# Kernel optimization log

Measured on AMD Instinct MI355X. Metric: run time of the kernel, lower is better.

## Reference

```python
import jax, jax.numpy as jnp
import numpy as np

B, L, D, E, H = 4, 2048, 512, 8, 1024

def setup_inputs() -> dict:
    key = jax.random.key(0)
    k1, k2, k3, k4 = jax.random.split(key, 4)
    x = jax.random.normal(k1, (B, L, D), dtype=jnp.float32)
    weights = jax.random.uniform(k2, (B, L, E), dtype=jnp.float32)
    w1 = jax.random.normal(k3, (E, D, H), dtype=jnp.float32) * 0.02
    b1 = jnp.zeros((E, H), dtype=jnp.float32)
    w2 = jax.random.normal(k4, (E, H, D), dtype=jnp.float32) * 0.02
    b2 = jnp.zeros((E, D), dtype=jnp.float32)
    return {"x": x, "weights": weights, "w1": w1, "b1": b1, "w2": w2, "b2": b2}

def reference(x, weights, w1, b1, w2, b2):
    # h: [B, L, E, H]
    h = jnp.einsum('bld,edh->bleh', x, w1) + b1[None, None, :, :]
    h = jax.nn.gelu(h, approximate=False)  # torch F.gelu default is exact (erf)
    # out: [B, L, E, D]
    out = jnp.einsum('bleh,ehd->bled', h, w2) + b2[None, None, :, :]
    # weighted sum over experts -> [B, L, D]
    return jnp.einsum('bled,ble->bld', out, weights)
```

## Files before the change

### kernel.cpp

```cpp
#include <hip/hip_runtime.h>
#include <hip/hip_bf16.h>

#define DEV __device__ __forceinline__

typedef __bf16 bf16;
typedef __bf16 bf16x4 __attribute__((ext_vector_type(4)));
typedef __bf16 bf16x8 __attribute__((ext_vector_type(8)));
typedef float f32x4 __attribute__((ext_vector_type(4)));

static constexpr int Bb = 4, Ll = 2048, Dd = 512, Ee = 8, Hh = 1024;
static constexpr int Mm = Bb * Ll;
static constexpr int GKS = Ee * Hh;

DEV void gload_lds16(const void* g, void* l) {
  __builtin_amdgcn_global_load_lds(
      (const __attribute__((address_space(1))) unsigned int*)g,
      (__attribute__((address_space(3))) unsigned int*)l, 16, 0, 0);
}

DEV float gelu_fast(float h) {
  const float k = 0.7978845608028654f * 2.0f * 1.4426950408889634f;
  float h2 = h * h;
  float y = h * (k + (0.044715f * k) * h2);
  float t = exp2f(y);
  return h - h * __frcp_rn(t + 1.0f);
}

__global__ void cvt_x_kernel(const float* __restrict__ in, bf16* __restrict__ out, int n4) {
  int i = blockIdx.x * blockDim.x + threadIdx.x;
  if (i < n4) {
    float4 v = ((const float4*)in)[i];
    bf16x4 o = {(bf16)v.x, (bf16)v.y, (bf16)v.z, (bf16)v.w};
    ((bf16x4*)out)[i] = o;
  }
}

__global__ void transpose_cvt(const float* __restrict__ in, bf16* __restrict__ out,
                              int R, int C, size_t in_es, size_t out_es, int out_rs) {
  __shared__ float tile[64][65];
  const int e = blockIdx.z;
  const float* ip = in + (size_t)e * in_es;
  bf16* op = out + (size_t)e * out_es;
  const int r0 = blockIdx.y * 64, c0 = blockIdx.x * 64;
  const int tc = threadIdx.x & 63, tr = threadIdx.x >> 6;
#pragma unroll
  for (int i = 0; i < 16; ++i) {
    const int r = tr + i * 4;
    tile[r][tc] = ip[(size_t)(r0 + r) * C + c0 + tc];
  }
  __syncthreads();
  const int wr = threadIdx.x & 63, wc0 = threadIdx.x >> 6;
#pragma unroll
  for (int i = 0; i < 16; ++i) {
    const int c = wc0 + i * 4;
    op[(size_t)(c0 + c) * out_rs + r0 + wr] = (bf16)tile[wr][c];
  }
}

template <int ARS, int BRS>
DEV void gemm256_core(const bf16* __restrict__ Ag, const bf16* __restrict__ Bg,
                      int nt, f32x4 (&acc)[8][4], char* lds) {
  const int t = threadIdx.x;
  const int lane = t & 63;
  const int wid = t >> 6;
  const int wm = wid >> 2, wn = wid & 3;
  const int fr = lane & 15, fg = lane >> 4;
  const int srow = t >> 3;
  const int sseg = t & 7;

  auto stage = [&](int kt, int p) {
    char* As = lds + p * 65536;
    char* Bs = lds + p * 65536 + 32768;
#pragma unroll
    for (int i = 0; i < 4; ++i) {
      const int row = i * 64 + srow;
      const int q = sseg ^ (row & 7);
      gload_lds16(Ag + (size_t)row * ARS + kt * 64 + q * 8, As + i * 8192 + wid * 1024);
      gload_lds16(Bg + (size_t)row * BRS + kt * 64 + q * 8, Bs + i * 8192 + wid * 1024);
    }
  };

  stage(0, 0);
  for (int kt = 0; kt < nt; ++kt) {
    const int p = kt & 1;
    if (kt + 1 < nt) {
      stage(kt + 1, p ^ 1);
      asm volatile("s_waitcnt vmcnt(8)" ::: "memory");
    } else {
      asm volatile("s_waitcnt vmcnt(0)" ::: "memory");
    }
    __builtin_amdgcn_s_barrier();
    const char* As = lds + p * 65536;
    const char* Bs = lds + p * 65536 + 32768;
    bf16x8 bfrag[4][2];
#pragma unroll
    for (int q = 0; q < 4; ++q) {
      if (q == 0) {
#pragma unroll
        for (int fj = 0; fj < 4; ++fj)
#pragma unroll
          for (int kk = 0; kk < 2; ++kk) {
            const int row = wn * 64 + fj * 16 + fr;
            const int seg = (kk * 4 + fg) ^ (row & 7);
            bfrag[fj][kk] = *(const bf16x8*)(Bs + row * 128 + seg * 16);
          }
      }
      bf16x8 af[2][2];
#pragma unroll
      for (int fil = 0; fil < 2; ++fil)
#pragma unroll
        for (int kk = 0; kk < 2; ++kk) {
          const int row = wm * 128 + (q * 2 + fil) * 16 + fr;
          const int seg = (kk * 4 + fg) ^ (row & 7);
          af[fil][kk] = *(const bf16x8*)(As + row * 128 + seg * 16);
        }
      __builtin_amdgcn_s_barrier();
      asm volatile("s_waitcnt lgkmcnt(0)" ::: "memory");
      __builtin_amdgcn_sched_barrier(0);
      __builtin_amdgcn_s_setprio(1);
#pragma unroll
      for (int fil = 0; fil < 2; ++fil)
#pragma unroll
        for (int fj = 0; fj < 4; ++fj)
#pragma unroll
          for (int kk = 0; kk < 2; ++kk)
            acc[q * 2 + fil][fj] = __builtin_amdgcn_mfma_f32_16x16x32_bf16(
                bfrag[fj][kk], af[fil][kk], acc[q * 2 + fil][fj], 0, 0, 0);
      __builtin_amdgcn_s_setprio(0);
      __builtin_amdgcn_s_barrier();
    }
  }
}

__global__ __launch_bounds__(512, 2) void ffn_stage1_256(
    const bf16* __restrict__ xb, const bf16* __restrict__ w1t,
    const float* __restrict__ b1, const float* __restrict__ wts,
    bf16* __restrict__ G) {
  __shared__ __align__(16) char lds[131072];
  __shared__ float b1s[256];
  __shared__ float wls[256];
  const int mt = blockIdx.x;
  const int e = blockIdx.y >> 2, ht2 = blockIdx.y & 3;
  const int t = threadIdx.x;
  if (t < 256) b1s[t] = b1[e * Hh + ht2 * 256 + t];
  else wls[t - 256] = wts[((size_t)mt * 256 + (t - 256)) * Ee + e];

  f32x4 acc[8][4] = {};
  const bf16* Ag = xb + (size_t)mt * 256 * Dd;
  const bf16* Bg = w1t + ((size_t)e * Hh + (size_t)ht2 * 256) * Dd;
  gemm256_core<Dd, Dd>(Ag, Bg, Dd / 64, acc, lds);

  const int lane = t & 63, wid = t >> 6;
  const int wm = wid >> 2, wn = wid & 3;
  const int fr = lane & 15, fq = lane >> 4;
  float b1v[4][4];
#pragma unroll
  for (int fj = 0; fj < 4; ++fj)
#pragma unroll
    for (int r = 0; r < 4; ++r) b1v[fj][r] = b1s[wn * 64 + fj * 16 + fq * 4 + r];
#pragma unroll
  for (int fi = 0; fi < 8; ++fi) {
    const int m = mt * 256 + wm * 128 + fi * 16 + fr;
    const float wgt = wls[wm * 128 + fi * 16 + fr];
    bf16* gp = G + (size_t)m * GKS + e * Hh + ht2 * 256 + wn * 64 + fq * 4;
#pragma unroll
    for (int fj = 0; fj < 4; ++fj) {
      bf16x4 o;
#pragma unroll
      for (int r = 0; r < 4; ++r) {
        float v = acc[fi][fj][r] + b1v[fj][r];
        o[r] = (bf16)(gelu_fast(v) * wgt);
      }
      *(bf16x4*)(gp + fj * 16) = o;
    }
  }
}

__global__ __launch_bounds__(512, 2) void ffn_stage2_256(
    const bf16* __restrict__ G, const bf16* __restrict__ w2t,
    float* __restrict__ P, int kchunk) {
  __shared__ __align__(16) char lds[131072];
  const int mt = blockIdx.x, nt = blockIdx.y, s = blockIdx.z;
  f32x4 acc[8][4] = {};
  const bf16* Ag = G + (size_t)mt * 256 * GKS + (size_t)s * kchunk;
  const bf16* Bg = w2t + (size_t)nt * 256 * GKS + (size_t)s * kchunk;
  gemm256_core<GKS, GKS>(Ag, Bg, kchunk / 64, acc, lds);

  float* Pp = P + (size_t)s * Mm * Dd;
  const int t = threadIdx.x;
  const int lane = t & 63, wid = t >> 6;
  const int wm = wid >> 2, wn = wid & 3;
  const int fr = lane & 15, fq = lane >> 4;
#pragma unroll
  for (int fi = 0; fi < 8; ++fi) {
    const size_t m = (size_t)mt * 256 + wm * 128 + fi * 16 + fr;
    float* pp = Pp + m * Dd + nt * 256 + wn * 64 + fq * 4;
#pragma unroll
    for (int fj = 0; fj < 4; ++fj) *(f32x4*)(pp + fj * 16) = acc[fi][fj];
  }
}

__global__ __launch_bounds__(256) void reduce_bias(
    const float* __restrict__ P, const float* __restrict__ wts,
    const float* __restrict__ b2, float* __restrict__ out, int S) {
  const int n4 = Mm * Dd / 4;
  int i = blockIdx.x * 256 + threadIdx.x;
  if (i >= n4) return;
  const int m = i / (Dd / 4);
  const int d0 = (i % (Dd / 4)) * 4;
  float4 a = ((const float4*)P)[i];
  for (int s = 1; s < S; ++s) {
    float4 p = ((const float4*)P)[(size_t)s * n4 + i];
    a.x += p.x; a.y += p.y; a.z += p.z; a.w += p.w;
  }
  const float* wr = wts + (size_t)m * Ee;
#pragma unroll
  for (int e = 0; e < Ee; ++e) {
    const float w = wr[e];
    float4 b = *(const float4*)(b2 + e * Dd + d0);
    a.x += w * b.x; a.y += w * b.y; a.z += w * b.z; a.w += w * b.w;
  }
  ((float4*)out)[i] = a;
}

template <int ARS, int BRS>
DEV void gemm_core(const bf16* __restrict__ Ag, const bf16* __restrict__ Bg,
                   int ksteps, f32x4 (&acc)[4][4], bf16* As, bf16* Bs) {
  const int t = threadIdx.x;
  const int lane = t & 63;
  const int w = t >> 6;
  const int srow = t >> 3;
  const int sseg = t & 7;
  const int wr = w >> 1, wc = w & 1;
  const int fr = lane & 15;
  const int fg = lane >> 4;
  for (int s = 0; s < ksteps; ++s) {
    __syncthreads();
#pragma unroll
    for (int i = 0; i < 4; ++i) {
      const int row = i * 32 + srow;
      const int q = sseg ^ (row & 7);
      gload_lds16(Ag + (size_t)row * ARS + s * 64 + q * 8,
                  (char*)As + i * 4096 + w * 1024);
      gload_lds16(Bg + (size_t)row * BRS + s * 64 + q * 8,
                  (char*)Bs + i * 4096 + w * 1024);
    }
    __syncthreads();
#pragma unroll
    for (int kk = 0; kk < 2; ++kk) {
      bf16x8 af[4], bfr[4];
#pragma unroll
      for (int mi = 0; mi < 4; ++mi) {
        const int row = wr * 64 + mi * 16 + fr;
        const int q = (kk * 4 + fg) ^ (row & 7);
        af[mi] = *(const bf16x8*)((const char*)As + row * 128 + q * 16);
      }
#pragma unroll
      for (int ni = 0; ni < 4; ++ni) {
        const int row = wc * 64 + ni * 16 + fr;
        const int q = (kk * 4 + fg) ^ (row & 7);
        bfr[ni] = *(const bf16x8*)((const char*)Bs + row * 128 + q * 16);
      }
#pragma unroll
      for (int mi = 0; mi < 4; ++mi)
#pragma unroll
        for (int ni = 0; ni < 4; ++ni)
          acc[mi][ni] = __builtin_amdgcn_mfma_f32_16x16x32_bf16(
              af[mi], bfr[ni], acc[mi][ni], 0, 0, 0);
    }
  }
}

__global__ __launch_bounds__(256) void ffn_stage1_t(
    const bf16* __restrict__ xb, const bf16* __restrict__ w1t,
    const float* __restrict__ b1, const float* __restrict__ wts,
    bf16* __restrict__ G) {
  __shared__ __align__(16) bf16 As[128 * 64];
  __shared__ __align__(16) bf16 Bs[128 * 64];
  __shared__ float b1s[128];
  __shared__ float wls[128];
  const int mt = blockIdx.x, ht = blockIdx.y, e = blockIdx.z;
  const int t = threadIdx.x;
  if (t < 128) b1s[t] = b1[e * Hh + ht * 128 + t];
  else wls[t - 128] = wts[((size_t)mt * 128 + (t - 128)) * Ee + e];
  f32x4 acc[4][4] = {};
  const bf16* Ag = xb + (size_t)mt * 128 * Dd;
  const bf16* Bg = w1t + ((size_t)e * Hh + (size_t)ht * 128) * Dd;
  gemm_core<Dd, Dd>(Ag, Bg, Dd / 64, acc, As, Bs);
  const int lane = t & 63, w = t >> 6;
  const int wr = w >> 1, wc = w & 1, fr = lane & 15, fq = lane >> 4;
  float bcol[4];
#pragma unroll
  for (int ni = 0; ni < 4; ++ni) bcol[ni] = b1s[wc * 64 + ni * 16 + fr];
  bf16* gp = G + ((size_t)mt * 128 + wr * 64 + fq * 4) * GKS
               + (size_t)e * Hh + ht * 128 + wc * 64 + fr;
#pragma unroll
  for (int mi = 0; mi < 4; ++mi)
#pragma unroll
    for (int r = 0; r < 4; ++r) {
      const float wgt = wls[wr * 64 + mi * 16 + fq * 4 + r];
#pragma unroll
      for (int ni = 0; ni < 4; ++ni) {
        float v = acc[mi][ni][r] + bcol[ni];
        gp[(size_t)(mi * 16 + r) * GKS + ni * 16] = (bf16)(gelu_fast(v) * wgt);
      }
    }
}

__global__ __launch_bounds__(256) void ffn_stage2_partial(
    const bf16* __restrict__ G, const bf16* __restrict__ w2t,
    float* __restrict__ P, int kchunk) {
  __shared__ __align__(16) bf16 As[128 * 64];
  __shared__ __align__(16) bf16 Bs[128 * 64];
  const int mt = blockIdx.x, nt = blockIdx.y, s = blockIdx.z;
  f32x4 acc[4][4] = {};
  const bf16* Ag = G + (size_t)mt * 128 * GKS + (size_t)s * kchunk;
  const bf16* Bg = w2t + (size_t)nt * 128 * GKS + (size_t)s * kchunk;
  gemm_core<GKS, GKS>(Ag, Bg, kchunk / 64, acc, As, Bs);
  float* Pp = P + (size_t)s * Mm * Dd;
  const int t = threadIdx.x;
  const int lane = t & 63, w = t >> 6;
  const int wr = w >> 1, wc = w & 1, fr = lane & 15, fq = lane >> 4;
#pragma unroll
  for (int mi = 0; mi < 4; ++mi)
#pragma unroll
    for (int r = 0; r < 4; ++r) {
      const size_t m = (size_t)mt * 128 + wr * 64 + mi * 16 + fq * 4 + r;
#pragma unroll
      for (int ni = 0; ni < 4; ++ni) {
        const int d = nt * 128 + wc * 64 + ni * 16 + fr;
        Pp[m * Dd + d] = acc[mi][ni][r];
      }
    }
}

extern "C" void kernel_launch(void* const* d_in, const int* in_sizes, int n_in,
                              void* d_out, int out_size, void* d_ws, size_t ws_size,
                              hipStream_t stream) {
  const float* x   = (const float*)d_in[0];
  const float* wts = (const float*)d_in[1];
  const float* w1  = (const float*)d_in[2];
  const float* b1  = (const float*)d_in[3];
  const float* w2  = (const float*)d_in[4];
  const float* b2  = (const float*)d_in[5];
  float* out = (float*)d_out;

  char* ws = (char*)d_ws;
  size_t off = 0;
  bf16* xb  = (bf16*)(ws + off); off += (size_t)Mm * Dd * 2;
  bf16* w1t = (bf16*)(ws + off); off += (size_t)Ee * Hh * Dd * 2;
  bf16* w2t = (bf16*)(ws + off); off += (size_t)Dd * Ee * Hh * 2;

  const size_t gfull = (size_t)Mm * Ee * Hh * 2;
  const size_t psz   = (size_t)Mm * Dd * 4;

  cvt_x_kernel<<<(Mm * Dd / 4 + 255) / 256, 256, 0, stream>>>(x, xb, Mm * Dd / 4);
  transpose_cvt<<<dim3(Hh / 64, Dd / 64, Ee), 256, 0, stream>>>(
      w1, w1t, Dd, Hh, (size_t)Dd * Hh, (size_t)Hh * Dd, Dd);
  transpose_cvt<<<dim3(Dd / 64, Hh / 64, Ee), 256, 0, stream>>>(
      w2, w2t, Hh, Dd, (size_t)Hh * Dd, (size_t)Hh, Ee * Hh);

  if (ws_size >= off + gfull + 4 * psz) {
    bf16* G = (bf16*)(ws + off);
    float* P = (float*)(ws + off + gfull);
    ffn_stage1_256<<<dim3(Mm / 256, (Ee * Hh) / 256), 512, 0, stream>>>(
        xb, w1t, b1, wts, G);
    ffn_stage2_256<<<dim3(Mm / 256, Dd / 256, 4), 512, 0, stream>>>(
        G, w2t, P, GKS / 4);
    reduce_bias<<<(Mm * Dd / 4 + 255) / 256, 256, 0, stream>>>(P, wts, b2, out, 4);
  } else if (ws_size >= off + gfull + 2 * psz) {
    bf16* G = (bf16*)(ws + off);
    float* P = (float*)(ws + off + gfull);
    ffn_stage1_t<<<dim3(Mm / 128, Hh / 128, Ee), 256, 0, stream>>>(
        xb, w1t, b1, wts, G);
    ffn_stage2_partial<<<dim3(Mm / 128, Dd / 128, 2), 256, 0, stream>>>(
        G, w2t, P, GKS / 2);
    reduce_bias<<<(Mm * Dd / 4 + 255) / 256, 256, 0, stream>>>(P, wts, b2, out, 2);
  }
}
```

Measured before the change: 220.9 us.

## Fuse four H tiles per block in stage1 into one continuous pipelined loop

Stage1 now processes all four 256-wide H tiles of an expert in one block. It runs a single 32-step double-buffered K loop and writes the GELU-weighted epilogue every 8 steps, so the load pipeline keeps going across tile boundaries and the block prologue is amortized. This cuts the grid to a quarter of the blocks, which lowers parallelism and can leave CUs idle. Stage2 inlines the former shared GEMM helper with no behavioural change.

After: 222.2 us. No clear change (+0.6%).

```diff
diff --git a/kernel.cpp b/kernel.cpp
--- a/kernel.cpp
+++ b/kernel.cpp
@@ -57,34 +57,49 @@
   }
 }
 
-template <int ARS, int BRS>
-DEV void gemm256_core(const bf16* __restrict__ Ag, const bf16* __restrict__ Bg,
-                      int nt, f32x4 (&acc)[8][4], char* lds) {
+__global__ __launch_bounds__(512, 2) void ffn_stage1_256(
+    const bf16* __restrict__ xb, const bf16* __restrict__ w1t,
+    const float* __restrict__ b1, const float* __restrict__ wts,
+    bf16* __restrict__ G) {
+  __shared__ __align__(16) char lds[131072];
+  __shared__ float b1s[1024];
+  __shared__ float wls[256];
+  const int mt = blockIdx.x, e = blockIdx.y;
   const int t = threadIdx.x;
+  b1s[t] = b1[e * Hh + t];
+  b1s[512 + t] = b1[e * Hh + 512 + t];
+  if (t < 256) wls[t] = wts[((size_t)mt * 256 + t) * Ee + e];
+
   const int lane = t & 63;
   const int wid = t >> 6;
   const int wm = wid >> 2, wn = wid & 3;
-  const int fr = lane & 15, fg = lane >> 4;
+  const int fr = lane & 15, fg = lane >> 4, fq = lane >> 4;
   const int srow = t >> 3;
   const int sseg = t & 7;
 
-  auto stage = [&](int kt, int p) {
+  const bf16* Ag = xb + (size_t)mt * 256 * Dd;
+  const bf16* Bg0 = w1t + (size_t)e * Hh * Dd;
+
+  auto stage = [&](int it, int p) {
+    const int ht2n = it >> 3, ktn = it & 7;
+    const bf16* Bg = Bg0 + (size_t)ht2n * 256 * Dd;
     char* As = lds + p * 65536;
     char* Bs = lds + p * 65536 + 32768;
 #pragma unroll
     for (int i = 0; i < 4; ++i) {
       const int row = i * 64 + srow;
       const int q = sseg ^ (row & 7);
-      gload_lds16(Ag + (size_t)row * ARS + kt * 64 + q * 8, As + i * 8192 + wid * 1024);
-      gload_lds16(Bg + (size_t)row * BRS + kt * 64 + q * 8, Bs + i * 8192 + wid * 1024);
+      gload_lds16(Ag + (size_t)row * Dd + ktn * 64 + q * 8, As + i * 8192 + wid * 1024);
+      gload_lds16(Bg + (size_t)row * Dd + ktn * 64 + q * 8, Bs + i * 8192 + wid * 1024);
     }
   };
 
+  f32x4 acc[8][4] = {};
   stage(0, 0);
-  for (int kt = 0; kt < nt; ++kt) {
-    const int p = kt & 1;
-    if (kt + 1 < nt) {
-      stage(kt + 1, p ^ 1);
+  for (int it = 0; it < 32; ++it) {
+    const int p = it & 1;
+    if (it + 1 < 32) {
+      stage(it + 1, p ^ 1);
       asm volatile("s_waitcnt vmcnt(8)" ::: "memory");
     } else {
       asm volatile("s_waitcnt vmcnt(0)" ::: "memory");
@@ -129,49 +144,32 @@
       __builtin_amdgcn_s_setprio(0);
       __builtin_amdgcn_s_barrier();
     }
-  }
-}
-
-__global__ __launch_bounds__(512, 2) void ffn_stage1_256(
-    const bf16* __restrict__ xb, const bf16* __restrict__ w1t,
-    const float* __restrict__ b1, const float* __restrict__ wts,
-    bf16* __restrict__ G) {
-  __shared__ __align__(16) char lds[131072];
-  __shared__ float b1s[256];
-  __shared__ float wls[256];
-  const int mt = blockIdx.x;
-  const int e = blockIdx.y >> 2, ht2 = blockIdx.y & 3;
-  const int t = threadIdx.x;
-  if (t < 256) b1s[t] = b1[e * Hh + ht2 * 256 + t];
-  else wls[t - 256] = wts[((size_t)mt * 256 + (t - 256)) * Ee + e];
-
-  f32x4 acc[8][4] = {};
-  const bf16* Ag = xb + (size_t)mt * 256 * Dd;
-  const bf16* Bg = w1t + ((size_t)e * Hh + (size_t)ht2 * 256) * Dd;
-  gemm256_core<Dd, Dd>(Ag, Bg, Dd / 64, acc, lds);
-
-  const int lane = t & 63, wid = t >> 6;
-  const int wm = wid >> 2, wn = wid & 3;
-  const int fr = lane & 15, fq = lane >> 4;
-  float b1v[4][4];
-#pragma unroll
-  for (int fj = 0; fj < 4; ++fj)
-#pragma unroll
-    for (int r = 0; r < 4; ++r) b1v[fj][r] = b1s[wn * 64 + fj * 16 + fq * 4 + r];
-#pragma unroll
-  for (int fi = 0; fi < 8; ++fi) {
-    const int m = mt * 256 + wm * 128 + fi * 16 + fr;
-    const float wgt = wls[wm * 128 + fi * 16 + fr];
-    bf16* gp = G + (size_t)m * GKS + e * Hh + ht2 * 256 + wn * 64 + fq * 4;
-#pragma unroll
-    for (int fj = 0; fj < 4; ++fj) {
-      bf16x4 o;
-#pragma unroll
-      for (int r = 0; r < 4; ++r) {
-        float v = acc[fi][fj][r] + b1v[fj][r];
-        o[r] = (bf16)(gelu_fast(v) * wgt);
-      }
-      *(bf16x4*)(gp + fj * 16) = o;
+    if ((it & 7) == 7) {
+      const int ht2 = it >> 3;
+      float b1v[4][4];
+#pragma unroll
+      for (int fj = 0; fj < 4; ++fj)
+#pragma unroll
+        for (int r = 0; r < 4; ++r)
+          b1v[fj][r] = b1s[ht2 * 256 + wn * 64 + fj * 16 + fq * 4 + r];
+#pragma unroll
+      for (int fi = 0; fi < 8; ++fi) {
+        const int m = mt * 256 + wm * 128 + fi * 16 + fr;
+        const float wgt = wls[wm * 128 + fi * 16 + fr];
+        bf16* gp = G + (size_t)m * GKS + e * Hh + ht2 * 256 + wn * 64 + fq * 4;
+#pragma unroll
+        for (int fj = 0; fj < 4; ++fj) {
+          bf16x4 o;
+#pragma unroll
+          for (int r = 0; r < 4; ++r) {
+            float v = acc[fi][fj][r] + b1v[fj][r];
+            o[r] = (bf16)(gelu_fast(v) * wgt);
+          }
+          *(bf16x4*)(gp + fj * 16) = o;
+        }
+#pragma unroll
+        for (int fj = 0; fj < 4; ++fj) acc[fi][fj] = (f32x4){0.f, 0.f, 0.f, 0.f};
+      }
     }
   }
 }
@@ -181,16 +179,84 @@
     float* __restrict__ P, int kchunk) {
   __shared__ __align__(16) char lds[131072];
   const int mt = blockIdx.x, nt = blockIdx.y, s = blockIdx.z;
-  f32x4 acc[8][4] = {};
+  const int t = threadIdx.x;
+  const int lane = t & 63;
+  const int wid = t >> 6;
+  const int wm = wid >> 2, wn = wid & 3;
+  const int fr = lane & 15, fg = lane >> 4;
+  const int srow = t >> 3;
+  const int sseg = t & 7;
+
   const bf16* Ag = G + (size_t)mt * 256 * GKS + (size_t)s * kchunk;
   const bf16* Bg = w2t + (size_t)nt * 256 * GKS + (size_t)s * kchunk;
-  gemm256_core<GKS, GKS>(Ag, Bg, kchunk / 64, acc, lds);
+
+  auto stage = [&](int kt, int p) {
+    char* As = lds + p * 65536;
+    char* Bs = lds + p * 65536 + 32768;
+#pragma unroll
+    for (int i = 0; i < 4; ++i) {
+      const int row = i * 64 + srow;
+      const int q = sseg ^ (row & 7);
+      gload_lds16(Ag + (size_t)row * GKS + kt * 64 + q * 8, As + i * 8192 + wid * 1024);
+      gload_lds16(Bg + (size_t)row * GKS + kt * 64 + q * 8, Bs + i * 8192 + wid * 1024);
+    }
+  };
+
+  f32x4 acc[8][4] = {};
+  const int nt_k = kchunk / 64;
+  stage(0, 0);
+  for (int kt = 0; kt < nt_k; ++kt) {
+    const int p = kt & 1;
+    if (kt + 1 < nt_k) {
+      stage(kt + 1, p ^ 1);
+      asm volatile("s_waitcnt vmcnt(8)" ::: "memory");
+    } else {
+      asm volatile("s_waitcnt vmcnt(0)" ::: "memory");
+    }
+    __builtin_amdgcn_s_barrier();
+    const char* As = lds + p * 65536;
+    const char* Bs = lds + p * 65536 + 32768;
+    bf16x8 bfrag[4][2];
+#pragma unroll
+    for (int q = 0; q < 4; ++q) {
+      if (q == 0) {
+#pragma unroll
+        for (int fj = 0; fj < 4; ++fj)
+#pragma unroll
+          for (int kk = 0; kk < 2; ++kk) {
+            const int row = wn * 64 + fj * 16 + fr;
+            const int seg = (kk * 4 + fg) ^ (row & 7);
+            bfrag[fj][kk] = *(const bf16x8*)(Bs + row * 128 + seg * 16);
+          }
+      }
+      bf16x8 af[2][2];
+#pragma unroll
+      for (int fil = 0; fil < 2; ++fil)
+#pragma unroll
+        for (int kk = 0; kk < 2; ++kk) {
+          const int row = wm * 128 + (q * 2 + fil) * 16 + fr;
+          const int seg = (kk * 4 + fg) ^ (row & 7);
+          af[fil][kk] = *(const bf16x8*)(As + row * 128 + seg * 16);
+        }
+      __builtin_amdgcn_s_barrier();
+      asm volatile("s_waitcnt lgkmcnt(0)" ::: "memory");
+      __builtin_amdgcn_sched_barrier(0);
+      __builtin_amdgcn_s_setprio(1);
+#pragma unroll
+      for (int fil = 0; fil < 2; ++fil)
+#pragma unroll
+        for (int fj = 0; fj < 4; ++fj)
+#pragma unroll
+          for (int kk = 0; kk < 2; ++kk)
+            acc[q * 2 + fil][fj] = __builtin_amdgcn_mfma_f32_16x16x32_bf16(
+                bfrag[fj][kk], af[fil][kk], acc[q * 2 + fil][fj], 0, 0, 0);
+      __builtin_amdgcn_s_setprio(0);
+      __builtin_amdgcn_s_barrier();
+    }
+  }
 
   float* Pp = P + (size_t)s * Mm * Dd;
-  const int t = threadIdx.x;
-  const int lane = t & 63, wid = t >> 6;
-  const int wm = wid >> 2, wn = wid & 3;
-  const int fr = lane & 15, fq = lane >> 4;
+  const int fq = lane >> 4;
 #pragma unroll
   for (int fi = 0; fi < 8; ++fi) {
     const size_t m = (size_t)mt * 256 + wm * 128 + fi * 16 + fr;
@@ -363,7 +429,7 @@
   if (ws_size >= off + gfull + 4 * psz) {
     bf16* G = (bf16*)(ws + off);
     float* P = (float*)(ws + off + gfull);
-    ffn_stage1_256<<<dim3(Mm / 256, (Ee * Hh) / 256), 512, 0, stream>>>(
+    ffn_stage1_256<<<dim3(Mm / 256, Ee), 512, 0, stream>>>(
         xb, w1t, b1, wts, G);
     ffn_stage2_256<<<dim3(Mm / 256, Dd / 256, 4), 512, 0, stream>>>(
         G, w2t, P, GKS / 4);
```

## Shrink GEMM tiles to 256x128 with K=32 steps for higher occupancy

Applied to the files above, without the earlier changes.

Replaces the 256x256 tile, K=64 GEMM core with a 256x128 tile and K=32 stages, using 8 waves in a 4x2 layout. Each wave now holds a 64x64 accumulator, and LDS use drops from 128KB to 48KB per block, so launch bounds are raised to 4 blocks per CU and the grids double along N. The aim is more blocks in flight and more latency hiding. In exchange, each tile reuses less data, global/LDS traffic per FLOP goes up, and there are more barriers per unit of K.

Measured after the change: 227.3 us. +2.9%, slower.

```diff
diff --git a/kernel.cpp b/kernel.cpp
--- a/kernel.cpp
+++ b/kernel.cpp
@@ -58,100 +58,88 @@
 }
 
 template <int ARS, int BRS>
-DEV void gemm256_core(const bf16* __restrict__ Ag, const bf16* __restrict__ Bg,
-                      int nt, f32x4 (&acc)[8][4], char* lds) {
+DEV void gemm128_run(const bf16* __restrict__ Ag, const bf16* __restrict__ Bg,
+                     int nt_k, f32x4 (&acc)[4][4], char* lds) {
   const int t = threadIdx.x;
   const int lane = t & 63;
   const int wid = t >> 6;
-  const int wm = wid >> 2, wn = wid & 3;
+  const int wm = wid >> 1, wn = wid & 1;
   const int fr = lane & 15, fg = lane >> 4;
-  const int srow = t >> 3;
-  const int sseg = t & 7;
+  const int srow = t >> 2;
+  const int sseg = t & 3;
 
   auto stage = [&](int kt, int p) {
-    char* As = lds + p * 65536;
-    char* Bs = lds + p * 65536 + 32768;
-#pragma unroll
-    for (int i = 0; i < 4; ++i) {
-      const int row = i * 64 + srow;
-      const int q = sseg ^ (row & 7);
-      gload_lds16(Ag + (size_t)row * ARS + kt * 64 + q * 8, As + i * 8192 + wid * 1024);
-      gload_lds16(Bg + (size_t)row * BRS + kt * 64 + q * 8, Bs + i * 8192 + wid * 1024);
+    char* As = lds + p * 24576;
+    char* Bs = lds + p * 24576 + 16384;
+#pragma unroll
+    for (int i = 0; i < 2; ++i) {
+      const int row = i * 128 + srow;
+      const int q = sseg ^ (row & 3);
+      gload_lds16(Ag + (size_t)row * ARS + kt * 32 + q * 8, As + i * 8192 + wid * 1024);
+    }
+    {
+      const int row = srow;
+      const int q = sseg ^ (row & 3);
+      gload_lds16(Bg + (size_t)row * BRS + kt * 32 + q * 8, Bs + wid * 1024);
     }
   };
 
   stage(0, 0);
-  for (int kt = 0; kt < nt; ++kt) {
+  for (int kt = 0; kt < nt_k; ++kt) {
     const int p = kt & 1;
-    if (kt + 1 < nt) {
+    if (kt + 1 < nt_k) {
       stage(kt + 1, p ^ 1);
-      asm volatile("s_waitcnt vmcnt(8)" ::: "memory");
+      asm volatile("s_waitcnt vmcnt(3)" ::: "memory");
     } else {
       asm volatile("s_waitcnt vmcnt(0)" ::: "memory");
     }
     __builtin_amdgcn_s_barrier();
-    const char* As = lds + p * 65536;
-    const char* Bs = lds + p * 65536 + 32768;
-    bf16x8 bfrag[4][2];
-#pragma unroll
-    for (int q = 0; q < 4; ++q) {
-      if (q == 0) {
-#pragma unroll
-        for (int fj = 0; fj < 4; ++fj)
-#pragma unroll
-          for (int kk = 0; kk < 2; ++kk) {
-            const int row = wn * 64 + fj * 16 + fr;
-            const int seg = (kk * 4 + fg) ^ (row & 7);
-            bfrag[fj][kk] = *(const bf16x8*)(Bs + row * 128 + seg * 16);
-          }
-      }
-      bf16x8 af[2][2];
-#pragma unroll
-      for (int fil = 0; fil < 2; ++fil)
-#pragma unroll
-        for (int kk = 0; kk < 2; ++kk) {
-          const int row = wm * 128 + (q * 2 + fil) * 16 + fr;
-          const int seg = (kk * 4 + fg) ^ (row & 7);
-          af[fil][kk] = *(const bf16x8*)(As + row * 128 + seg * 16);
-        }
-      __builtin_amdgcn_s_barrier();
-      asm volatile("s_waitcnt lgkmcnt(0)" ::: "memory");
-      __builtin_amdgcn_sched_barrier(0);
-      __builtin_amdgcn_s_setprio(1);
-#pragma unroll
-      for (int fil = 0; fil < 2; ++fil)
-#pragma unroll
-        for (int fj = 0; fj < 4; ++fj)
-#pragma unroll
-          for (int kk = 0; kk < 2; ++kk)
-            acc[q * 2 + fil][fj] = __builtin_amdgcn_mfma_f32_16x16x32_bf16(
-                bfrag[fj][kk], af[fil][kk], acc[q * 2 + fil][fj], 0, 0, 0);
-      __builtin_amdgcn_s_setprio(0);
-      __builtin_amdgcn_s_barrier();
-    }
-  }
-}
-
-__global__ __launch_bounds__(512, 2) void ffn_stage1_256(
+    const char* As = lds + p * 24576;
+    const char* Bs = lds + p * 24576 + 16384;
+    bf16x8 bfr[4], af[4];
+#pragma unroll
+    for (int fj = 0; fj < 4; ++fj) {
+      const int row = wn * 64 + fj * 16 + fr;
+      const int s = fg ^ (row & 3);
+      bfr[fj] = *(const bf16x8*)(Bs + row * 64 + s * 16);
+    }
+#pragma unroll
+    for (int fi = 0; fi < 4; ++fi) {
+      const int row = wm * 64 + fi * 16 + fr;
+      const int s = fg ^ (row & 3);
+      af[fi] = *(const bf16x8*)(As + row * 64 + s * 16);
+    }
+    __builtin_amdgcn_s_setprio(1);
+#pragma unroll
+    for (int fi = 0; fi < 4; ++fi)
+#pragma unroll
+      for (int fj = 0; fj < 4; ++fj)
+        acc[fi][fj] = __builtin_amdgcn_mfma_f32_16x16x32_bf16(
+            bfr[fj], af[fi], acc[fi][fj], 0, 0, 0);
+    __builtin_amdgcn_s_setprio(0);
+    __builtin_amdgcn_s_barrier();
+  }
+}
+
+__global__ __launch_bounds__(512, 4) void ffn_stage1_256(
     const bf16* __restrict__ xb, const bf16* __restrict__ w1t,
     const float* __restrict__ b1, const float* __restrict__ wts,
     bf16* __restrict__ G) {
-  __shared__ __align__(16) char lds[131072];
-  __shared__ float b1s[256];
+  __shared__ __align__(16) char lds[49152];
+  __shared__ float b1s[128];
   __shared__ float wls[256];
-  const int mt = blockIdx.x;
-  const int e = blockIdx.y >> 2, ht2 = blockIdx.y & 3;
-  const int t = threadIdx.x;
-  if (t < 256) b1s[t] = b1[e * Hh + ht2 * 256 + t];
-  else wls[t - 256] = wts[((size_t)mt * 256 + (t - 256)) * Ee + e];
-
-  f32x4 acc[8][4] = {};
+  const int mt = blockIdx.x, ct = blockIdx.y;
+  const int t = threadIdx.x;
+  if (t < 128) b1s[t] = b1[ct * 128 + t];
+  else if (t < 384) wls[t - 128] = wts[((size_t)mt * 256 + (t - 128)) * Ee + (ct >> 3)];
+
+  f32x4 acc[4][4] = {};
   const bf16* Ag = xb + (size_t)mt * 256 * Dd;
-  const bf16* Bg = w1t + ((size_t)e * Hh + (size_t)ht2 * 256) * Dd;
-  gemm256_core<Dd, Dd>(Ag, Bg, Dd / 64, acc, lds);
+  const bf16* Bg = w1t + (size_t)ct * 128 * Dd;
+  gemm128_run<Dd, Dd>(Ag, Bg, Dd / 32, acc, lds);
 
   const int lane = t & 63, wid = t >> 6;
-  const int wm = wid >> 2, wn = wid & 3;
+  const int wm = wid >> 1, wn = wid & 1;
   const int fr = lane & 15, fq = lane >> 4;
   float b1v[4][4];
 #pragma unroll
@@ -159,10 +147,10 @@
 #pragma unroll
     for (int r = 0; r < 4; ++r) b1v[fj][r] = b1s[wn * 64 + fj * 16 + fq * 4 + r];
 #pragma unroll
-  for (int fi = 0; fi < 8; ++fi) {
-    const int m = mt * 256 + wm * 128 + fi * 16 + fr;
-    const float wgt = wls[wm * 128 + fi * 16 + fr];
-    bf16* gp = G + (size_t)m * GKS + e * Hh + ht2 * 256 + wn * 64 + fq * 4;
+  for (int fi = 0; fi < 4; ++fi) {
+    const int m = mt * 256 + wm * 64 + fi * 16 + fr;
+    const float wgt = wls[wm * 64 + fi * 16 + fr];
+    bf16* gp = G + (size_t)m * GKS + ct * 128 + wn * 64 + fq * 4;
 #pragma unroll
     for (int fj = 0; fj < 4; ++fj) {
       bf16x4 o;
@@ -176,25 +164,26 @@
   }
 }
 
-__global__ __launch_bounds__(512, 2) void ffn_stage2_256(
+__global__ __launch_bounds__(512, 4) void ffn_stage2_256(
     const bf16* __restrict__ G, const bf16* __restrict__ w2t,
     float* __restrict__ P, int kchunk) {
-  __shared__ __align__(16) char lds[131072];
+  __shared__ __align__(16) char lds[49152];
   const int mt = blockIdx.x, nt = blockIdx.y, s = blockIdx.z;
-  f32x4 acc[8][4] = {};
+  const int t = threadIdx.x;
+
+  f32x4 acc[4][4] = {};
   const bf16* Ag = G + (size_t)mt * 256 * GKS + (size_t)s * kchunk;
-  const bf16* Bg = w2t + (size_t)nt * 256 * GKS + (size_t)s * kchunk;
-  gemm256_core<GKS, GKS>(Ag, Bg, kchunk / 64, acc, lds);
+  const bf16* Bg = w2t + (size_t)nt * 128 * GKS + (size_t)s * kchunk;
+  gemm128_run<GKS, GKS>(Ag, Bg, kchunk / 32, acc, lds);
 
   float* Pp = P + (size_t)s * Mm * Dd;
-  const int t = threadIdx.x;
   const int lane = t & 63, wid = t >> 6;
-  const int wm = wid >> 2, wn = wid & 3;
+  const int wm = wid >> 1, wn = wid & 1;
   const int fr = lane & 15, fq = lane >> 4;
 #pragma unroll
-  for (int fi = 0; fi < 8; ++fi) {
-    const size_t m = (size_t)mt * 256 + wm * 128 + fi * 16 + fr;
-    float* pp = Pp + m * Dd + nt * 256 + wn * 64 + fq * 4;
+  for (int fi = 0; fi < 4; ++fi) {
+    const size_t m = (size_t)mt * 256 + wm * 64 + fi * 16 + fr;
+    float* pp = Pp + m * Dd + nt * 128 + wn * 64 + fq * 4;
 #pragma unroll
     for (int fj = 0; fj < 4; ++fj) *(f32x4*)(pp + fj * 16) = acc[fi][fj];
   }
@@ -363,9 +352,9 @@
   if (ws_size >= off + gfull + 4 * psz) {
     bf16* G = (bf16*)(ws + off);
     float* P = (float*)(ws + off + gfull);
-    ffn_stage1_256<<<dim3(Mm / 256, (Ee * Hh) / 256), 512, 0, stream>>>(
+    ffn_stage1_256<<<dim3(Mm / 256, GKS / 128), 512, 0, stream>>>(
         xb, w1t, b1, wts, G);
-    ffn_stage2_256<<<dim3(Mm / 256, Dd / 256, 4), 512, 0, stream>>>(
+    ffn_stage2_256<<<dim3(Mm / 256, Dd / 128, 4), 512, 0, stream>>>(
         G, w2t, P, GKS / 4);
     reduce_bias<<<(Mm * Dd / 4 + 255) / 256, 256, 0, stream>>>(P, wts, b2, out, 4);
   } else if (ws_size >= off + gfull + 2 * psz) {
```

## Restructure GEMM pipeline to triple-buffered K=32 stages with interleaved loads

Applied to the files above, without the earlier changes.

Replaces the shared double-buffered K=64 GEMM core with a triple-buffered K=32 pipeline. The next tile's A and B global-to-LDS loads are issued between the two MFMA clusters, and the LDS swizzle is changed to match the narrower rows. Stage 1 now has each block loop over all four 256-wide H tiles of one expert in a single persistent loop, writing the GELU epilogue every 16 iterations. This cuts the grid from 1024 to 256 blocks and lets the pipeline run without a drain between tiles. Launch bounds drop from 2 to 1 block per CU, trading occupancy for deeper prefetch and fewer load stalls.

Result: no change. 223.9 us (+1.3%).

```diff
diff --git a/kernel.cpp b/kernel.cpp
--- a/kernel.cpp
+++ b/kernel.cpp
@@ -57,140 +57,168 @@
   }
 }
 
-template <int ARS, int BRS>
-DEV void gemm256_core(const bf16* __restrict__ Ag, const bf16* __restrict__ Bg,
-                      int nt, f32x4 (&acc)[8][4], char* lds) {
-  const int t = threadIdx.x;
-  const int lane = t & 63;
-  const int wid = t >> 6;
-  const int wm = wid >> 2, wn = wid & 3;
-  const int fr = lane & 15, fg = lane >> 4;
-  const int srow = t >> 3;
-  const int sseg = t & 7;
-
-  auto stage = [&](int kt, int p) {
-    char* As = lds + p * 65536;
-    char* Bs = lds + p * 65536 + 32768;
-#pragma unroll
-    for (int i = 0; i < 4; ++i) {
-      const int row = i * 64 + srow;
-      const int q = sseg ^ (row & 7);
-      gload_lds16(Ag + (size_t)row * ARS + kt * 64 + q * 8, As + i * 8192 + wid * 1024);
-      gload_lds16(Bg + (size_t)row * BRS + kt * 64 + q * 8, Bs + i * 8192 + wid * 1024);
-    }
-  };
-
-  stage(0, 0);
-  for (int kt = 0; kt < nt; ++kt) {
-    const int p = kt & 1;
-    if (kt + 1 < nt) {
-      stage(kt + 1, p ^ 1);
-      asm volatile("s_waitcnt vmcnt(8)" ::: "memory");
-    } else {
-      asm volatile("s_waitcnt vmcnt(0)" ::: "memory");
-    }
-    __builtin_amdgcn_s_barrier();
-    const char* As = lds + p * 65536;
-    const char* Bs = lds + p * 65536 + 32768;
-    bf16x8 bfrag[4][2];
-#pragma unroll
-    for (int q = 0; q < 4; ++q) {
-      if (q == 0) {
-#pragma unroll
-        for (int fj = 0; fj < 4; ++fj)
-#pragma unroll
-          for (int kk = 0; kk < 2; ++kk) {
-            const int row = wn * 64 + fj * 16 + fr;
-            const int seg = (kk * 4 + fg) ^ (row & 7);
-            bfrag[fj][kk] = *(const bf16x8*)(Bs + row * 128 + seg * 16);
-          }
-      }
-      bf16x8 af[2][2];
-#pragma unroll
-      for (int fil = 0; fil < 2; ++fil)
-#pragma unroll
-        for (int kk = 0; kk < 2; ++kk) {
-          const int row = wm * 128 + (q * 2 + fil) * 16 + fr;
-          const int seg = (kk * 4 + fg) ^ (row & 7);
-          af[fil][kk] = *(const bf16x8*)(As + row * 128 + seg * 16);
-        }
-      __builtin_amdgcn_s_barrier();
-      asm volatile("s_waitcnt lgkmcnt(0)" ::: "memory");
-      __builtin_amdgcn_sched_barrier(0);
-      __builtin_amdgcn_s_setprio(1);
-#pragma unroll
-      for (int fil = 0; fil < 2; ++fil)
-#pragma unroll
-        for (int fj = 0; fj < 4; ++fj)
-#pragma unroll
-          for (int kk = 0; kk < 2; ++kk)
-            acc[q * 2 + fil][fj] = __builtin_amdgcn_mfma_f32_16x16x32_bf16(
-                bfrag[fj][kk], af[fil][kk], acc[q * 2 + fil][fj], 0, 0, 0);
-      __builtin_amdgcn_s_setprio(0);
-      __builtin_amdgcn_s_barrier();
-    }
-  }
-}
-
-__global__ __launch_bounds__(512, 2) void ffn_stage1_256(
+#define PIPE_DECLS                                                   \
+  const int t = threadIdx.x;                                         \
+  const int lane = t & 63;                                           \
+  const int wid = t >> 6;                                            \
+  const int wm = wid >> 2, wn = wid & 3;                             \
+  const int fr = lane & 15, fg = lane >> 4, fq = lane >> 4;          \
+  const int srow = t >> 2;                                           \
+  const int sq = (t & 3) ^ ((t >> 3) & 3);                           \
+  const int rsl = fg ^ ((fr >> 1) & 3);
+
+#define PHASE0(buf)                                                  \
+  bf16x8 bfr[4], af[4];                                              \
+  _Pragma("unroll") for (int fj = 0; fj < 4; ++fj) {                 \
+    const int row = wn * 64 + fj * 16 + fr;                          \
+    bfr[fj] = *(const bf16x8*)((buf) + 16384 + row * 64 + rsl * 16); \
+  }                                                                  \
+  _Pragma("unroll") for (int fi = 0; fi < 4; ++fi) {                 \
+    const int row = wm * 128 + fi * 16 + fr;                         \
+    af[fi] = *(const bf16x8*)((buf) + row * 64 + rsl * 16);          \
+  }
+
+#define PHASE1_READS(buf)                                            \
+  bf16x8 af2[4];                                                     \
+  _Pragma("unroll") for (int fi = 0; fi < 4; ++fi) {                 \
+    const int row = wm * 128 + (4 + fi) * 16 + fr;                   \
+    af2[fi] = *(const bf16x8*)((buf) + row * 64 + rsl * 16);         \
+  }
+
+#define MFMA_CLUSTER(A, ACCOFF)                                      \
+  __builtin_amdgcn_s_barrier();                                      \
+  asm volatile("s_waitcnt lgkmcnt(0)" ::: "memory");                 \
+  __builtin_amdgcn_sched_barrier(0);                                 \
+  __builtin_amdgcn_s_setprio(1);                                     \
+  _Pragma("unroll") for (int fi = 0; fi < 4; ++fi)                   \
+  _Pragma("unroll") for (int fj = 0; fj < 4; ++fj)                   \
+    acc[(ACCOFF) + fi][fj] = __builtin_amdgcn_mfma_f32_16x16x32_bf16(\
+        bfr[fj], (A)[fi], acc[(ACCOFF) + fi][fj], 0, 0, 0);          \
+  __builtin_amdgcn_s_setprio(0);
+
+__global__ __launch_bounds__(512, 1) void ffn_stage1_f(
     const bf16* __restrict__ xb, const bf16* __restrict__ w1t,
     const float* __restrict__ b1, const float* __restrict__ wts,
     bf16* __restrict__ G) {
-  __shared__ __align__(16) char lds[131072];
-  __shared__ float b1s[256];
+  __shared__ __align__(16) char lds[98304];
+  __shared__ float b1s[1024];
   __shared__ float wls[256];
-  const int mt = blockIdx.x;
-  const int e = blockIdx.y >> 2, ht2 = blockIdx.y & 3;
-  const int t = threadIdx.x;
-  if (t < 256) b1s[t] = b1[e * Hh + ht2 * 256 + t];
-  else wls[t - 256] = wts[((size_t)mt * 256 + (t - 256)) * Ee + e];
+  const int mt = blockIdx.x, e = blockIdx.y;
+  PIPE_DECLS
+  b1s[t] = b1[e * Hh + t];
+  b1s[512 + t] = b1[e * Hh + 512 + t];
+  if (t < 256) wls[t] = wts[((size_t)mt * 256 + t) * Ee + e];
+
+  const bf16* Ag = xb + (size_t)mt * 256 * Dd;
+  const bf16* Bg0 = w1t + (size_t)e * Hh * Dd;
+
+  auto stageA = [&](int it, char* buf) {
+    const int k0 = (it & 15) * 32;
+    gload_lds16(Ag + (size_t)srow * Dd + k0 + sq * 8, buf + wid * 1024);
+    gload_lds16(Ag + (size_t)(128 + srow) * Dd + k0 + sq * 8, buf + 8192 + wid * 1024);
+  };
+  auto stageB = [&](int it, char* buf) {
+    const bf16* Bg = Bg0 + (size_t)(it >> 4) * 256 * Dd;
+    const int k0 = (it & 15) * 32;
+    gload_lds16(Bg + (size_t)srow * Dd + k0 + sq * 8, buf + 16384 + wid * 1024);
+    gload_lds16(Bg + (size_t)(128 + srow) * Dd + k0 + sq * 8, buf + 24576 + wid * 1024);
+  };
 
   f32x4 acc[8][4] = {};
-  const bf16* Ag = xb + (size_t)mt * 256 * Dd;
-  const bf16* Bg = w1t + ((size_t)e * Hh + (size_t)ht2 * 256) * Dd;
-  gemm256_core<Dd, Dd>(Ag, Bg, Dd / 64, acc, lds);
-
-  const int lane = t & 63, wid = t >> 6;
-  const int wm = wid >> 2, wn = wid & 3;
-  const int fr = lane & 15, fq = lane >> 4;
-  float b1v[4][4];
-#pragma unroll
-  for (int fj = 0; fj < 4; ++fj)
-#pragma unroll
-    for (int r = 0; r < 4; ++r) b1v[fj][r] = b1s[wn * 64 + fj * 16 + fq * 4 + r];
-#pragma unroll
-  for (int fi = 0; fi < 8; ++fi) {
-    const int m = mt * 256 + wm * 128 + fi * 16 + fr;
-    const float wgt = wls[wm * 128 + fi * 16 + fr];
-    bf16* gp = G + (size_t)m * GKS + e * Hh + ht2 * 256 + wn * 64 + fq * 4;
-#pragma unroll
-    for (int fj = 0; fj < 4; ++fj) {
-      bf16x4 o;
-#pragma unroll
-      for (int r = 0; r < 4; ++r) {
-        float v = acc[fi][fj][r] + b1v[fj][r];
-        o[r] = (bf16)(gelu_fast(v) * wgt);
+  const int NT = 64;
+  stageA(0, lds); stageB(0, lds);
+  stageA(1, lds + 32768); stageB(1, lds + 32768);
+  for (int it = 0; it < NT; ++it) {
+    char* buf = lds + (it % 3) * 32768;
+    char* nbuf = lds + ((it + 2) % 3) * 32768;
+    if (it + 1 < NT) {
+      asm volatile("s_waitcnt vmcnt(4)" ::: "memory");
+    } else {
+      asm volatile("s_waitcnt vmcnt(0)" ::: "memory");
+    }
+    __builtin_amdgcn_s_barrier();
+    {
+      PHASE0(buf)
+      if (it + 2 < NT) stageA(it + 2, nbuf);
+      MFMA_CLUSTER(af, 0)
+      PHASE1_READS(buf)
+      if (it + 2 < NT) stageB(it + 2, nbuf);
+      MFMA_CLUSTER(af2, 4)
+    }
+    if ((it & 15) == 15) {
+      const int ct = it >> 4;
+      float b1v[4][4];
+#pragma unroll
+      for (int fj = 0; fj < 4; ++fj)
+#pragma unroll
+        for (int r = 0; r < 4; ++r)
+          b1v[fj][r] = b1s[ct * 256 + wn * 64 + fj * 16 + fq * 4 + r];
+#pragma unroll
+      for (int fi = 0; fi < 8; ++fi) {
+        const int m = mt * 256 + wm * 128 + fi * 16 + fr;
+        const float wgt = wls[wm * 128 + fi * 16 + fr];
+        bf16* gp = G + (size_t)m * GKS + e * Hh + ct * 256 + wn * 64 + fq * 4;
+#pragma unroll
+        for (int fj = 0; fj < 4; ++fj) {
+          bf16x4 o;
+#pragma unroll
+          for (int r = 0; r < 4; ++r) {
+            float v = acc[fi][fj][r] + b1v[fj][r];
+            o[r] = (bf16)(gelu_fast(v) * wgt);
+          }
+          *(bf16x4*)(gp + fj * 16) = o;
+#pragma unroll
+          for (int r = 0; r < 4; ++r) acc[fi][fj][r] = 0.f;
+        }
       }
-      *(bf16x4*)(gp + fj * 16) = o;
-    }
-  }
-}
-
-__global__ __launch_bounds__(512, 2) void ffn_stage2_256(
+    }
+  }
+}
+
+__global__ __launch_bounds__(512, 1) void ffn_stage2_f(
     const bf16* __restrict__ G, const bf16* __restrict__ w2t,
-    float* __restrict__ P, int kchunk) {
-  __shared__ __align__(16) char lds[131072];
+    float* __restrict__ P) {
+  __shared__ __align__(16) char lds[98304];
   const int mt = blockIdx.x, nt = blockIdx.y, s = blockIdx.z;
+  PIPE_DECLS
+  const bf16* Ag = G + (size_t)mt * 256 * GKS + (size_t)s * 2048;
+  const bf16* Bg = w2t + (size_t)nt * 256 * GKS + (size_t)s * 2048;
+
+  auto stageA = [&](int it, char* buf) {
+    const int k0 = it * 32;
+    gload_lds16(Ag + (size_t)srow * GKS + k0 + sq * 8, buf + wid * 1024);
+    gload_lds16(Ag + (size_t)(128 + srow) * GKS + k0 + sq * 8, buf + 8192 + wid * 1024);
+  };
+  auto stageB = [&](int it, char* buf) {
+    const int k0 = it * 32;
+    gload_lds16(Bg + (size_t)srow * GKS + k0 + sq * 8, buf + 16384 + wid * 1024);
+    gload_lds16(Bg + (size_t)(128 + srow) * GKS + k0 + sq * 8, buf + 24576 + wid * 1024);
+  };
+
   f32x4 acc[8][4] = {};
-  const bf16* Ag = G + (size_t)mt * 256 * GKS + (size_t)s * kchunk;
-  const bf16* Bg = w2t + (size_t)nt * 256 * GKS + (size_t)s * kchunk;
-  gemm256_core<GKS, GKS>(Ag, Bg, kchunk / 64, acc, lds);
+  const int NT = 64;
+  stageA(0, lds); stageB(0, lds);
+  stageA(1, lds + 32768); stageB(1, lds + 32768);
+  for (int it = 0; it < NT; ++it) {
+    char* buf = lds + (it % 3) * 32768;
+    char* nbuf = lds + ((it + 2) % 3) * 32768;
+    if (it + 1 < NT) {
+      asm volatile("s_waitcnt vmcnt(4)" ::: "memory");
+    } else {
+      asm volatile("s_waitcnt vmcnt(0)" ::: "memory");
+    }
+    __builtin_amdgcn_s_barrier();
+    {
+      PHASE0(buf)
+      if (it + 2 < NT) stageA(it + 2, nbuf);
+      MFMA_CLUSTER(af, 0)
+      PHASE1_READS(buf)
+      if (it + 2 < NT) stageB(it + 2, nbuf);
+      MFMA_CLUSTER(af2, 4)
+    }
+  }
 
   float* Pp = P + (size_t)s * Mm * Dd;
-  const int t = threadIdx.x;
-  const int lane = t & 63, wid = t >> 6;
-  const int wm = wid >> 2, wn = wid & 3;
-  const int fr = lane & 15, fq = lane >> 4;
 #pragma unroll
   for (int fi = 0; fi < 8; ++fi) {
     const size_t m = (size_t)mt * 256 + wm * 128 + fi * 16 + fr;
@@ -363,10 +391,10 @@
   if (ws_size >= off + gfull + 4 * psz) {
     bf16* G = (bf16*)(ws + off);
     float* P = (float*)(ws + off + gfull);
-    ffn_stage1_256<<<dim3(Mm / 256, (Ee * Hh) / 256), 512, 0, stream>>>(
+    ffn_stage1_f<<<dim3(Mm / 256, Ee), 512, 0, stream>>>(
         xb, w1t, b1, wts, G);
-    ffn_stage2_256<<<dim3(Mm / 256, Dd / 256, 4), 512, 0, stream>>>(
-        G, w2t, P, GKS / 4);
+    ffn_stage2_f<<<dim3(Mm / 256, Dd / 256, 4), 512, 0, stream>>>(
+        G, w2t, P);
     reduce_bias<<<(Mm * Dd / 4 + 255) / 256, 256, 0, stream>>>(P, wts, b2, out, 4);
   } else if (ws_size >= off + gfull + 2 * psz) {
     bf16* G = (bf16*)(ws + off);
```
